# Kernel tuning notes

Measured on AMD Instinct MI355X. Metric: run time of the kernel, lower is better.

## Reference

```python
import jax, jax.numpy as jnp
import numpy as np

BRANCH = 4
DEPTH = 5
D = 512
N_NODES = (BRANCH ** (DEPTH + 1) - 1) // (BRANCH - 1)  # 1365
BATCH = 16


def setup_inputs() -> dict:
    key = jax.random.key(0)
    k1, k2, k3 = jax.random.split(key, 3)
    inputs = jax.random.normal(k1, (BATCH, D), dtype=jnp.float32)
    # per-node Linear(512,512) weights, torch layout [out, in], scaled like kaiming-ish init
    W = jax.random.normal(k2, (N_NODES, D, D), dtype=jnp.float32) * (1.0 / np.sqrt(D))
    b = jax.random.normal(k3, (N_NODES, D), dtype=jnp.float32) * 0.01
    return {"inputs": inputs, "W": W, "b": b}


def reference(inputs, W, b):
    # BFS over a complete BRANCH-ary tree; node i>0 has parent (i-1)//BRANCH.
    # Root: Linear only (no relu, per source); children: relu(Linear(parent_act)).
    # All nodes at one BFS level are batched into a single grouped einsum.
    acts = []
    a = inputs @ W[0].T + b[0]          # [B, D] root, no relu
    acts.append(a[:, None, :])
    prev = acts[0]                       # [B, level_size, D]
    prev_start = 0
    start = 1
    for lvl in range(1, DEPTH + 1):
        sz = BRANCH ** lvl
        idx = np.arange(start, start + sz)
        parent_local = (idx - 1) // BRANCH - prev_start  # indices into prev level
        pa = prev[:, parent_local, :]                    # [B, sz, D]
        Wl = W[start:start + sz]                         # [sz, D(out), D(in)]
        bl = b[start:start + sz]                         # [sz, D]
        a = jax.nn.relu(jnp.einsum('bnd,nhd->bnh', pa, Wl) + bl)  # [B, sz, D]
        acts.append(a)
        prev = a
        prev_start = start
        start += sz
    out = jnp.concatenate(acts, axis=1)                  # [B, N_NODES, D]
    return out.reshape(out.shape[0], -1)                 # [B, N_NODES*D], like torch.cat(dim=1)
```

## Files before the change

kernel.cpp:

```cpp
#include <hip/hip_runtime.h>

#define D 512
#define NNODES 1365
#define OUT_STRIDE (NNODES * D)

typedef __attribute__((ext_vector_type(4))) float f32x4;
typedef __attribute__((ext_vector_type(8))) short bf16x8;

union U4 { uint4 q; unsigned u[4]; bf16x8 v; };

__device__ inline unsigned cvt_pk_bf16(float s0, float s1) {
    unsigned r;
    asm volatile("v_cvt_pk_bf16_f32 %0, %1, %2" : "=v"(r) : "v"(s0), "v"(s1));
    return r;
}

__device__ inline void gld_lds16(const void* g, void* l) {
    __builtin_amdgcn_global_load_lds(
        (const __attribute__((address_space(1))) unsigned*)g,
        (__attribute__((address_space(3))) unsigned*)l, 16, 0, 0);
}

template<int NC, bool RELU>
__global__ __launch_bounds__(256, 2)
void node_kernel(const float* __restrict__ W,
                 const float* __restrict__ bias,
                 const float* __restrict__ src_base,
                 float* __restrict__ out,
                 int node_start, int bpn, int src_stride)
{
    __shared__ float Wt[4][2][2048];

    const int tid  = threadIdx.x;
    const int w    = tid >> 6;
    const int lane = tid & 63;
    const int m4   = lane >> 4;
    const int c0   = lane & 15;

    const int node  = node_start + blockIdx.x / bpn;
    const int nbase = (blockIdx.x % bpn) * (16 * NC);
    const float* Wn = W + (size_t)node * (D * D);

    const int drow = ((lane >> 2) & 1) + 2 * ((lane >> 3) & 1);
    const int loff = drow * 2048 +
        ((lane >> 5) * 8 + (lane & 3) * 2 + ((lane >> 4) & 1)) * 16;

    auto issue_chunk = [&](int c) {
        const char* gsrc = (const char*)Wn +
            (size_t)(nbase + (c * 4 + w) * 4) * 2048 + loff;
        char* ldst = (char*)&Wt[w][c & 1][0];
        #pragma unroll
        for (int i = 0; i < 8; ++i)
            gld_lds16(gsrc + i * 256, ldst + i * 1024);
    };

    float bf[NC];
    #pragma unroll
    for (int c = 0; c < NC; ++c) {
        bf[c] = bias[(size_t)node * D + nbase + (c * 4 + w) * 4 + (c0 & 3)];
        asm volatile("" :: "v"(bf[c]));
    }

    const float* arow = (RELU ? src_base + (size_t)((node - 1) >> 2) * D
                              : src_base) + (size_t)c0 * src_stride;
    bf16x8 aH[16], aL[16];
    #pragma unroll
    for (int j = 0; j < 16; ++j) {
        const float* p = arow + j * 32 + m4 * 8;
        float4 x0 = *(const float4*)p;
        float4 x1 = *(const float4*)(p + 4);
        float xs[8] = {x0.x,x0.y,x0.z,x0.w,x1.x,x1.y,x1.z,x1.w};
        U4 h, l;
        #pragma unroll
        for (int k = 0; k < 4; ++k) {
            unsigned hh = cvt_pk_bf16(xs[2*k], xs[2*k+1]);
            float f0 = __uint_as_float(hh << 16);
            float f1 = __uint_as_float(hh & 0xFFFF0000u);
            l.u[k] = cvt_pk_bf16(xs[2*k] - f0, xs[2*k+1] - f1);
            h.u[k] = hh;
        }
        aH[j] = h.v; aL[j] = l.v;
    }

    issue_chunk(0);
    if (NC > 1) issue_chunk(1);

    const int laneoff = ((c0 >> 1) & 1) * 128 + (c0 & 1) * 64 + m4 * 16;

    #pragma unroll
    for (int c = 0; c < NC; ++c) {
        if      (c == NC - 1) asm volatile("s_waitcnt vmcnt(0)"  ::: "memory");
        else if (c == 0)      asm volatile("s_waitcnt vmcnt(8)"  ::: "memory");
        else if (c == 1)      asm volatile("s_waitcnt vmcnt(12)" ::: "memory");
        else                  asm volatile("s_waitcnt vmcnt(16)" ::: "memory");

        const char* tb = (const char*)&Wt[w][c & 1][0];
        f32x4 acc = {0.f, 0.f, 0.f, 0.f};
        #pragma unroll
        for (int ks = 0; ks < 16; ++ks) {
            float4 b0 = *(const float4*)(tb + ks * 512 + laneoff);
            float4 b1 = *(const float4*)(tb + ks * 512 + laneoff + 256);
            U4 bH, bL;
            float xs[8] = {b0.x,b0.y,b0.z,b0.w,b1.x,b1.y,b1.z,b1.w};
            #pragma unroll
            for (int k = 0; k < 4; ++k) {
                unsigned hh = cvt_pk_bf16(xs[2*k], xs[2*k+1]);
                float f0 = __uint_as_float(hh << 16);
                float f1 = __uint_as_float(hh & 0xFFFF0000u);
                bL.u[k] = cvt_pk_bf16(xs[2*k] - f0, xs[2*k+1] - f1);
                bH.u[k] = hh;
            }
            acc = __builtin_amdgcn_mfma_f32_16x16x32_bf16(aH[ks], bH.v, acc, 0,0,0);
            acc = __builtin_amdgcn_mfma_f32_16x16x32_bf16(aL[ks], bH.v, acc, 0,0,0);
            acc = __builtin_amdgcn_mfma_f32_16x16x32_bf16(aH[ks], bL.v, acc, 0,0,0);
        }

        if (c + 2 < NC) issue_chunk(c + 2);

        if (c0 < 4) {
            const int wcol = node * D + nbase + (c * 4 + w) * 4 + c0;
            const float bv = bf[c];
            #pragma unroll
            for (int i = 0; i < 4; ++i) {
                float v = acc[i] + bv;
                if (RELU) v = fmaxf(v, 0.f);
                out[(size_t)(m4 * 4 + i) * OUT_STRIDE + wcol] = v;
            }
        }
    }
}

extern "C" void kernel_launch(void* const* d_in, const int* in_sizes, int n_in,
                              void* d_out, int out_size, void* d_ws, size_t ws_size,
                              hipStream_t stream) {
    const float* inputs = (const float*)d_in[0];
    const float* W      = (const float*)d_in[1];
    const float* bias   = (const float*)d_in[2];
    float* out          = (float*)d_out;

    node_kernel<1, false><<<  32, 256, 0, stream>>>(W, bias, inputs, out,   0, 32, D);
    node_kernel<1, true ><<< 128, 256, 0, stream>>>(W, bias, out,    out,   1, 32, OUT_STRIDE);
    node_kernel<2, true ><<< 256, 256, 0, stream>>>(W, bias, out,    out,   5, 16, OUT_STRIDE);
    node_kernel<4, true ><<< 512, 256, 0, stream>>>(W, bias, out,    out,  21,  8, OUT_STRIDE);
    node_kernel<8, true ><<<1024, 256, 0, stream>>>(W, bias, out,    out,  85,  4, OUT_STRIDE);
    node_kernel<8, true ><<<4096, 256, 0, stream>>>(W, bias, out,    out, 341,  4, OUT_STRIDE);
}
```

Measured before the change: 428.7 us.

## Restructure weight tiling: 16-column wave groups, XOR-swizzled LDS, runtime group loop

Each wave now loads 16 contiguous output rows of W, reading full 2KB rows split into four K-quarters. These are double-buffered through LDS with an XOR swizzle, replacing the earlier 4-column chunks. Bias is staged in LDS, stores write 16 contiguous columns, and a runtime loop over column groups lets each block cover more of a node, so grids are smaller on the deep levels. The aim is more coalesced global loads and stores, fewer LDS bank conflicts, and a finer K-level pipeline. The trade-off is fewer blocks on the large levels (e.g. 1024 instead of 4096), which may reduce latency hiding.

```diff
diff --git a/kernel.cpp b/kernel.cpp
--- a/kernel.cpp
+++ b/kernel.cpp
@@ -21,15 +21,16 @@
         (__attribute__((address_space(3))) unsigned*)l, 16, 0, 0);
 }
 
-template<int NC, bool RELU>
+template<bool RELU>
 __global__ __launch_bounds__(256, 2)
 void node_kernel(const float* __restrict__ W,
                  const float* __restrict__ bias,
                  const float* __restrict__ src_base,
                  float* __restrict__ out,
-                 int node_start, int bpn, int src_stride)
+                 int node_start, int bpn, int ngroups, int src_stride)
 {
     __shared__ float Wt[4][2][2048];
+    __shared__ float bias_lds[512];
 
     const int tid  = threadIdx.x;
     const int w    = tid >> 6;
@@ -38,28 +39,11 @@
     const int c0   = lane & 15;
 
     const int node  = node_start + blockIdx.x / bpn;
-    const int nbase = (blockIdx.x % bpn) * (16 * NC);
-    const float* Wn = W + (size_t)node * (D * D);
+    const int nbase = (blockIdx.x % bpn) * (64 * ngroups);
+    const char* Wn  = (const char*)(W + (size_t)node * (D * D));
 
-    const int drow = ((lane >> 2) & 1) + 2 * ((lane >> 3) & 1);
-    const int loff = drow * 2048 +
-        ((lane >> 5) * 8 + (lane & 3) * 2 + ((lane >> 4) & 1)) * 16;
-
-    auto issue_chunk = [&](int c) {
-        const char* gsrc = (const char*)Wn +
-            (size_t)(nbase + (c * 4 + w) * 4) * 2048 + loff;
-        char* ldst = (char*)&Wt[w][c & 1][0];
-        #pragma unroll
-        for (int i = 0; i < 8; ++i)
-            gld_lds16(gsrc + i * 256, ldst + i * 1024);
-    };
-
-    float bf[NC];
-    #pragma unroll
-    for (int c = 0; c < NC; ++c) {
-        bf[c] = bias[(size_t)node * D + nbase + (c * 4 + w) * 4 + (c0 & 3)];
-        asm volatile("" :: "v"(bf[c]));
-    }
+    for (int t = tid; t < 64 * ngroups; t += 256)
+        bias_lds[t] = bias[(size_t)node * D + nbase + t];
 
     const float* arow = (RELU ? src_base + (size_t)((node - 1) >> 2) * D
                               : src_base) + (size_t)c0 * src_stride;
@@ -81,25 +65,43 @@
         }
         aH[j] = h.v; aL[j] = l.v;
     }
+    __syncthreads();
 
-    issue_chunk(0);
-    if (NC > 1) issue_chunk(1);
+    int loffs[8];
+    const int rr  = lane >> 5;
+    const int off = (lane & 31) * 16;
+    #pragma unroll
+    for (int i = 0; i < 8; ++i) {
+        const int r = i * 2 + rr;
+        loffs[i] = r * 2048 + (off ^ ((r & 7) << 4));
+    }
 
-    const int laneoff = ((c0 >> 1) & 1) * 128 + (c0 & 1) * 64 + m4 * 16;
+    auto issue = [&](const char* gsrc, int buf) {
+        char* ldst = (char*)&Wt[w][buf][0];
+        #pragma unroll
+        for (int i = 0; i < 8; ++i)
+            gld_lds16(gsrc + loffs[i], ldst + i * 1024);
+    };
 
-    #pragma unroll
-    for (int c = 0; c < NC; ++c) {
-        if      (c == NC - 1) asm volatile("s_waitcnt vmcnt(0)"  ::: "memory");
-        else if (c == 0)      asm volatile("s_waitcnt vmcnt(8)"  ::: "memory");
-        else if (c == 1)      asm volatile("s_waitcnt vmcnt(12)" ::: "memory");
-        else                  asm volatile("s_waitcnt vmcnt(16)" ::: "memory");
+    const int rsw = (c0 & 7) << 4;
+    const int po0 = c0 * 512 + ((m4 * 32)      ^ rsw);
+    const int po1 = c0 * 512 + ((m4 * 32 + 16) ^ rsw);
 
-        const char* tb = (const char*)&Wt[w][c & 1][0];
-        f32x4 acc = {0.f, 0.f, 0.f, 0.f};
+    const size_t GRP = (size_t)64 * 2048;
+    const char* gcur = Wn + (size_t)(nbase + w * 16) * 2048;
+    issue(gcur,       0);
+    issue(gcur + 512, 1);
+
+    float* optr = out + (size_t)node * D + nbase + w * 16 + c0;
+    const float* blds = &bias_lds[w * 16 + c0];
+
+    auto compute_q = [&](auto qc, f32x4& acc) {
+        constexpr int Q = decltype(qc)::value;
+        const char* tb = (const char*)&Wt[w][Q & 1][0];
         #pragma unroll
-        for (int ks = 0; ks < 16; ++ks) {
-            float4 b0 = *(const float4*)(tb + ks * 512 + laneoff);
-            float4 b1 = *(const float4*)(tb + ks * 512 + laneoff + 256);
+        for (int ks = 0; ks < 4; ++ks) {
+            float4 b0 = *(const float4*)(tb + po0 + ks * 128);
+            float4 b1 = *(const float4*)(tb + po1 + ks * 128);
             U4 bH, bL;
             float xs[8] = {b0.x,b0.y,b0.z,b0.w,b1.x,b1.y,b1.z,b1.w};
             #pragma unroll
@@ -110,23 +112,41 @@
                 bL.u[k] = cvt_pk_bf16(xs[2*k] - f0, xs[2*k+1] - f1);
                 bH.u[k] = hh;
             }
-            acc = __builtin_amdgcn_mfma_f32_16x16x32_bf16(aH[ks], bH.v, acc, 0,0,0);
-            acc = __builtin_amdgcn_mfma_f32_16x16x32_bf16(aL[ks], bH.v, acc, 0,0,0);
-            acc = __builtin_amdgcn_mfma_f32_16x16x32_bf16(aH[ks], bL.v, acc, 0,0,0);
+            acc = __builtin_amdgcn_mfma_f32_16x16x32_bf16(aH[Q*4+ks], bH.v, acc, 0,0,0);
+            acc = __builtin_amdgcn_mfma_f32_16x16x32_bf16(aL[Q*4+ks], bH.v, acc, 0,0,0);
+            acc = __builtin_amdgcn_mfma_f32_16x16x32_bf16(aH[Q*4+ks], bL.v, acc, 0,0,0);
         }
+    };
 
-        if (c + 2 < NC) issue_chunk(c + 2);
+    #pragma clang loop unroll(disable)
+    for (int g = 0; g < ngroups; ++g) {
+        const bool last = (g == ngroups - 1);
+        const char* gnext = gcur + GRP;
+        f32x4 acc = {0.f, 0.f, 0.f, 0.f};
 
-        if (c0 < 4) {
-            const int wcol = node * D + nbase + (c * 4 + w) * 4 + c0;
-            const float bv = bf[c];
-            #pragma unroll
-            for (int i = 0; i < 4; ++i) {
-                float v = acc[i] + bv;
-                if (RELU) v = fmaxf(v, 0.f);
-                out[(size_t)(m4 * 4 + i) * OUT_STRIDE + wcol] = v;
-            }
+        asm volatile("s_waitcnt vmcnt(8)" ::: "memory");
+        compute_q(std::integral_constant<int,0>{}, acc);
+        issue(gcur + 1024, 0);
+        asm volatile("s_waitcnt vmcnt(8)" ::: "memory");
+        compute_q(std::integral_constant<int,1>{}, acc);
+        issue(gcur + 1536, 1);
+        asm volatile("s_waitcnt vmcnt(8)" ::: "memory");
+        compute_q(std::integral_constant<int,2>{}, acc);
+        if (!last) issue(gnext, 0);
+        if (last) asm volatile("s_waitcnt vmcnt(0)" ::: "memory");
+        else      asm volatile("s_waitcnt vmcnt(8)" ::: "memory");
+        compute_q(std::integral_constant<int,3>{}, acc);
+
+        const float bv = *blds;
+        #pragma unroll
+        for (int i = 0; i < 4; ++i) {
+            float v = acc[i] + bv;
+            if (RELU) v = fmaxf(v, 0.f);
+            optr[(size_t)(m4 * 4 + i) * OUT_STRIDE] = v;
         }
+        if (!last) issue(gnext + 512, 1);
+
+        gcur = gnext; optr += 64; blds += 64;
     }
 }
 
@@ -138,10 +158,10 @@
     const float* bias   = (const float*)d_in[2];
     float* out          = (float*)d_out;
 
-    node_kernel<1, false><<<  32, 256, 0, stream>>>(W, bias, inputs, out,   0, 32, D);
-    node_kernel<1, true ><<< 128, 256, 0, stream>>>(W, bias, out,    out,   1, 32, OUT_STRIDE);
-    node_kernel<2, true ><<< 256, 256, 0, stream>>>(W, bias, out,    out,   5, 16, OUT_STRIDE);
-    node_kernel<4, true ><<< 512, 256, 0, stream>>>(W, bias, out,    out,  21,  8, OUT_STRIDE);
-    node_kernel<8, true ><<<1024, 256, 0, stream>>>(W, bias, out,    out,  85,  4, OUT_STRIDE);
-    node_kernel<8, true ><<<4096, 256, 0, stream>>>(W, bias, out,    out, 341,  4, OUT_STRIDE);
+    node_kernel<false><<<   8, 256, 0, stream>>>(W, bias, inputs, out,   0, 8, 1, D);
+    node_kernel<true ><<<  32, 256, 0, stream>>>(W, bias, out,    out,   1, 8, 1, OUT_STRIDE);
+    node_kernel<true ><<< 128, 256, 0, stream>>>(W, bias, out,    out,   5, 8, 1, OUT_STRIDE);
+    node_kernel<true ><<< 512, 256, 0, stream>>>(W, bias, out,    out,  21, 8, 1, OUT_STRIDE);
+    node_kernel<true ><<< 512, 256, 0, stream>>>(W, bias, out,    out,  85, 2, 4, OUT_STRIDE);
+    node_kernel<true ><<<1024, 256, 0, stream>>>(W, bias, out,    out, 341, 1, 8, OUT_STRIDE);
 }
```

Result: faster. 346.3 us (-19.2%).
